# Optimization experiments

Hardware: AMD Instinct MI355X
Metric: run time of the kernel (lower is better)

Reference implementation:

```python
import jax, jax.numpy as jnp
import numpy as np

H = 128   # LSTM hidden size
E = 300   # embedding dim
PAD_ID = 0
UNK_ID = 1


def _lstm_dir(x, Wih, Whh, b):
    """Single-direction LSTM. x: [B,S,E] -> hidden states [B,S,H]. PyTorch gate order i,f,g,o."""
    B = x.shape[0]
    def step(carry, xt):
        h, c = carry
        g = xt @ Wih.T + h @ Whh.T + b            # [B,4H]
        i, f, gg, o = jnp.split(g, 4, axis=-1)
        c = jax.nn.sigmoid(f) * c + jax.nn.sigmoid(i) * jnp.tanh(gg)
        h = jax.nn.sigmoid(o) * jnp.tanh(c)
        return (h, c), h
    init = (jnp.zeros((B, H), x.dtype), jnp.zeros((B, H), x.dtype))
    _, hs = jax.lax.scan(step, init, jnp.swapaxes(x, 0, 1))   # [S,B,H]
    return jnp.swapaxes(hs, 0, 1)


def setup_inputs() -> dict:
    key = jax.random.key(0)
    ks = jax.random.split(key, 12)
    B, S, D = 32, 512, 8
    WORD_V, DEP_V, NUM_LABELS = 100000, 64, 5
    inp = {
        "word_ids": jax.random.randint(ks[0], (B, 3, S), 0, WORD_V, dtype=jnp.int32),
        "deps_ids": jax.random.randint(ks[1], (B, S, D), 0, DEP_V, dtype=jnp.int32),
        "word_table": jax.random.normal(ks[2], (WORD_V, E), jnp.float32) * 0.1,
        "dep_table": jax.random.normal(ks[3], (DEP_V, E), jnp.float32) * 0.1,
        "Wih_f": jax.random.normal(ks[4], (4 * H, E), jnp.float32) * 0.05,
        "Whh_f": jax.random.normal(ks[5], (4 * H, H), jnp.float32) * 0.05,
        "b_f": jnp.zeros((4 * H,), jnp.float32),
        "Wih_b": jax.random.normal(ks[6], (4 * H, E), jnp.float32) * 0.05,
        "Whh_b": jax.random.normal(ks[7], (4 * H, H), jnp.float32) * 0.05,
        "b_b": jnp.zeros((4 * H,), jnp.float32),
        "W_cls": jax.random.normal(ks[8], (NUM_LABELS, 2 * H), jnp.float32) * 0.05,
        "b_cls": jnp.zeros((NUM_LABELS,), jnp.float32),
    }
    return inp


def reference(word_ids, deps_ids, word_table, dep_table,
              Wih_f, Whh_f, b_f, Wih_b, Whh_b, b_b, W_cls, b_cls):
    # word_ids[:, 1, :] -> token ids used for word embeddings
    word_embs = word_table[word_ids[:, 1, :]]          # [B,S,E]
    dep_embs = dep_table[deps_ids]                     # [B,S,D,E]

    # vectorized masked mean-pool of dep embeddings (skip pad/unk ids)
    mask = ((deps_ids != PAD_ID) & (deps_ids != UNK_ID)).astype(word_embs.dtype)[..., None]  # [B,S,D,1]
    cnt = mask.sum(axis=2)                             # [B,S,1]
    dep_mean = (dep_embs * mask).sum(axis=2) / jnp.maximum(cnt, 1.0)
    word_embs = jnp.where(cnt > 0, 0.5 * word_embs + 0.5 * dep_mean, word_embs)

    # BiLSTM
    out_f = _lstm_dir(word_embs, Wih_f, Whh_f, b_f)                       # [B,S,H]
    out_b = _lstm_dir(word_embs[:, ::-1, :], Wih_b, Whh_b, b_b)[:, ::-1, :]
    out = jnp.concatenate([out_f, out_b], axis=-1)                        # [B,S,2H]

    # max-pool over time, dropout is identity in eval, then classifier
    pooled = out.max(axis=1)                           # [B,2H]
    logits = pooled @ W_cls.T + b_cls                  # [B,num_labels]
    return logits
```

## Files before the change

### kernel.cpp

```cpp
#include <hip/hip_runtime.h>
#include <hip/hip_bf16.h>
#include <cstdint>
#include <cstddef>

#define S_LEN 512
#define BATCH 32
#define EDIM  300
#define KPAD  320
#define K3    960
#define HDIM  128
#define NGATE 512
#define NCOLS 1024

typedef float    f2  __attribute__((ext_vector_type(2)));
typedef float    f4v __attribute__((ext_vector_type(4)));
typedef short    short8 __attribute__((ext_vector_type(8)));
typedef _Float16 h2  __attribute__((ext_vector_type(2)));

__device__ __forceinline__ float sigm_fast(float x) {
    return __builtin_amdgcn_rcpf(1.f + __expf(-x));
}
__device__ __forceinline__ float tanh_fast(float x) {
    return 2.f * sigm_fast(2.f * x) - 1.f;
}

template <int CTRL>
__device__ __forceinline__ float dpp_mov(float x) {
    int r = __builtin_amdgcn_update_dpp(0, __float_as_int(x), CTRL, 0xF, 0xF, true);
    return __int_as_float(r);
}

__device__ __forceinline__ h2 pk_f16(float a, float b) {
    auto r = __builtin_amdgcn_cvt_pkrtz(a, b);
    return __builtin_bit_cast(h2, r);
}

__device__ __forceinline__ void bf16_split(float v, ushort& hi, ushort& lo) {
    __hip_bfloat16 hb = __float2bfloat16(v);
    float hf = __bfloat162float(hb);
    __hip_bfloat16 lb = __float2bfloat16(v - hf);
    hi = *reinterpret_cast<ushort*>(&hb);
    lo = *reinterpret_cast<ushort*>(&lb);
}

__global__ void embed_xcat(const int* __restrict__ word_ids,
                           const int* __restrict__ deps_ids,
                           const float* __restrict__ word_table,
                           const float* __restrict__ dep_table,
                           ushort* __restrict__ Xcat) {
    int pos = blockIdx.x;
    int b = pos >> 9, s = pos & (S_LEN - 1);
    int wid = word_ids[b * 3 * S_LEN + S_LEN + s];
    const int* dp = deps_ids + (size_t)pos * 8;
    int ids[8];
    int cnt = 0;
#pragma unroll
    for (int d = 0; d < 8; ++d) {
        int id = dp[d];
        ids[d] = id;
        cnt += (id != 0 && id != 1) ? 1 : 0;
    }
    float inv = 0.5f / (float)((cnt > 0) ? cnt : 1);
    const float* wr = word_table + (size_t)wid * EDIM;
    ushort* xr = Xcat + (size_t)pos * K3;
    for (int e = threadIdx.x; e < KPAD; e += 128) {
        float v = 0.f;
        if (e < EDIM) {
            float w = wr[e];
            float dsum = 0.f;
#pragma unroll
            for (int d = 0; d < 8; ++d) {
                if (ids[d] != 0 && ids[d] != 1) dsum += dep_table[ids[d] * EDIM + e];
            }
            v = (cnt > 0) ? (0.5f * w + dsum * inv) : w;
        }
        ushort hu, lu;
        bf16_split(v, hu, lu);
        xr[e] = hu;
        xr[KPAD + e] = hu;
        xr[2 * KPAD + e] = lu;
    }
}

__global__ void wcat_kernel(const float* __restrict__ Wih_f,
                            const float* __restrict__ Wih_b,
                            ushort* __restrict__ Wcat) {
    int n = blockIdx.x;
    const float* src = (n < NGATE) ? (Wih_f + (size_t)n * EDIM)
                                   : (Wih_b + (size_t)(n - NGATE) * EDIM);
    ushort* wr = Wcat + (size_t)n * K3;
    for (int e = threadIdx.x; e < KPAD; e += 128) {
        float v = (e < EDIM) ? src[e] : 0.f;
        ushort hu, lu;
        bf16_split(v, hu, lu);
        wr[e] = hu;
        wr[KPAD + e] = lu;
        wr[2 * KPAD + e] = hu;
    }
}

#define LSTR 40
__global__ __launch_bounds__(256) void gemm_mfma(
        const ushort* __restrict__ Xcat,
        const ushort* __restrict__ Wcat,
        const float* __restrict__ b_f, const float* __restrict__ b_b,
        float* __restrict__ pre) {
    __shared__ ushort Asub[128 * LSTR];
    __shared__ ushort Bsub[128 * LSTR];
    int tid = threadIdx.x;
    int wave = tid >> 6, lane = tid & 63;
    int lid = lane & 15, quad = lane >> 4;
    int m0 = blockIdx.x * 128, n0 = blockIdx.y * 128;
    int wm = (wave >> 1) * 64, wn = (wave & 1) * 64;

    f4v acc[4][4];
#pragma unroll
    for (int i = 0; i < 4; ++i)
#pragma unroll
        for (int j = 0; j < 4; ++j) acc[i][j] = (f4v)0.f;

    float bias[4];
#pragma unroll
    for (int nt = 0; nt < 4; ++nt) {
        int n = n0 + wn + nt * 16 + lid;
        bias[nt] = (n < NGATE) ? b_f[n] : b_b[n - NGATE];
    }

    int c0 = tid, c1 = tid + 256;
    const ushort* aptr0 = Xcat + (size_t)(m0 + (c0 >> 2)) * K3 + (c0 & 3) * 8;
    const ushort* aptr1 = Xcat + (size_t)(m0 + (c1 >> 2)) * K3 + (c1 & 3) * 8;
    const ushort* bptr0 = Wcat + (size_t)(n0 + (c0 >> 2)) * K3 + (c0 & 3) * 8;
    const ushort* bptr1 = Wcat + (size_t)(n0 + (c1 >> 2)) * K3 + (c1 & 3) * 8;
    int la0 = (c0 >> 2) * LSTR + (c0 & 3) * 8;
    int la1 = (c1 >> 2) * LSTR + (c1 & 3) * 8;

    short8 ra0 = *(const short8*)(aptr0);
    short8 ra1 = *(const short8*)(aptr1);
    short8 rb0 = *(const short8*)(bptr0);
    short8 rb1 = *(const short8*)(bptr1);

    for (int k0 = 0; k0 < K3; k0 += 32) {
        __syncthreads();
        *(short8*)&Asub[la0] = ra0;
        *(short8*)&Asub[la1] = ra1;
        *(short8*)&Bsub[la0] = rb0;
        *(short8*)&Bsub[la1] = rb1;
        __syncthreads();
        if (k0 + 32 < K3) {
            ra0 = *(const short8*)(aptr0 + k0 + 32);
            ra1 = *(const short8*)(aptr1 + k0 + 32);
            rb0 = *(const short8*)(bptr0 + k0 + 32);
            rb1 = *(const short8*)(bptr1 + k0 + 32);
        }
        short8 aF[4], bF[4];
#pragma unroll
        for (int mt = 0; mt < 4; ++mt)
            aF[mt] = *(const short8*)&Asub[(wm + mt * 16 + lid) * LSTR + quad * 8];
#pragma unroll
        for (int nt = 0; nt < 4; ++nt)
            bF[nt] = *(const short8*)&Bsub[(wn + nt * 16 + lid) * LSTR + quad * 8];
#pragma unroll
        for (int mt = 0; mt < 4; ++mt)
#pragma unroll
            for (int nt = 0; nt < 4; ++nt)
                acc[mt][nt] = __builtin_amdgcn_mfma_f32_16x16x32_bf16(
                    aF[mt], bF[nt], acc[mt][nt], 0, 0, 0);
    }

#pragma unroll
    for (int mt = 0; mt < 4; ++mt)
#pragma unroll
        for (int nt = 0; nt < 4; ++nt) {
            int n = n0 + wn + nt * 16 + lid;
#pragma unroll
            for (int r = 0; r < 4; ++r) {
                int m = m0 + wm + mt * 16 + quad * 4 + r;
                pre[(size_t)m * NCOLS + n] = acc[mt][nt][r] + bias[nt];
            }
        }
}

__global__ __launch_bounds__(256, 1) void lstm_rec(
        const float* __restrict__ pre,
        const float* __restrict__ Whh_f, const float* __restrict__ Whh_b,
        float* __restrict__ pooled) {
    __shared__ _Float16 h_s[HDIM];
    int t = threadIdx.x;
    int lane = t & 63;
    int wv = t >> 6;
    int tau = lane & 3;
    int hx0 = wv * 16 + (lane >> 2);
    int hx1 = hx0 + 64;
    int b = blockIdx.x >> 1;
    int dir = blockIdx.x & 1;
    const float* Whh = dir ? Whh_b : Whh_f;

    h2 w0[64], w1[64];
    {
        const float* r0 = Whh + (size_t)(tau * HDIM + hx0) * HDIM;
        const float* r1 = Whh + (size_t)(tau * HDIM + hx1) * HDIM;
#pragma unroll
        for (int q = 0; q < 64; ++q) {
            w0[q] = pk_f16(r0[2 * q], r0[2 * q + 1]);
            w1[q] = pk_f16(r1[2 * q], r1[2 * q + 1]);
        }
    }

    float c0 = 0.f, c1 = 0.f;
    float hmax0 = -1e30f, hmax1 = -1e30f;
    if (t < 64) ((uint*)h_s)[t] = 0u;

    const float* pb0 = pre + (size_t)b * S_LEN * NCOLS + dir * NGATE + tau * HDIM + hx0;
    const float* pb1 = pb0 + 64;
    int s = dir ? (S_LEN - 1) : 0;
    int ds = dir ? -1 : 1;
    float p0n1 = pb0[(long)s * NCOLS];
    float p1n1 = pb1[(long)s * NCOLS];
    float p0n2 = pb0[(long)(s + ds) * NCOLS];
    float p1n2 = pb1[(long)(s + ds) * NCOLS];

    asm volatile("s_waitcnt lgkmcnt(0)\n\ts_barrier" ::: "memory");

    for (int step = 0; step < S_LEN; ++step) {
        float cur0 = p0n1, cur1 = p1n1;
        p0n1 = p0n2; p1n1 = p1n2;
        if (step + 2 < S_LEN) {
            p0n2 = pb0[(long)(s + 2 * ds) * NCOLS];
            p1n2 = pb1[(long)(s + 2 * ds) * NCOLS];
        }

        h2 hh[64];
        const h2* hp = (const h2*)h_s;
#pragma unroll
        for (int q = 0; q < 64; ++q) hh[q] = hp[q];

        float a0 = 0.f, a1 = 0.f, a2 = 0.f, a3 = 0.f;
        float e0 = 0.f, e1 = 0.f, e2 = 0.f, e3 = 0.f;
#pragma unroll
        for (int q = 0; q < 64; q += 4) {
            a0 = __builtin_amdgcn_fdot2(w0[q + 0], hh[q + 0], a0, false);
            a1 = __builtin_amdgcn_fdot2(w0[q + 1], hh[q + 1], a1, false);
            a2 = __builtin_amdgcn_fdot2(w0[q + 2], hh[q + 2], a2, false);
            a3 = __builtin_amdgcn_fdot2(w0[q + 3], hh[q + 3], a3, false);
            e0 = __builtin_amdgcn_fdot2(w1[q + 0], hh[q + 0], e0, false);
            e1 = __builtin_amdgcn_fdot2(w1[q + 1], hh[q + 1], e1, false);
            e2 = __builtin_amdgcn_fdot2(w1[q + 2], hh[q + 2], e2, false);
            e3 = __builtin_amdgcn_fdot2(w1[q + 3], hh[q + 3], e3, false);
        }
        float g0 = cur0 + (a0 + a1) + (a2 + a3);
        float g1 = cur1 + (e0 + e1) + (e2 + e3);

        float gi0 = dpp_mov<0x00>(g0), gf0 = dpp_mov<0x55>(g0);
        float gg0 = dpp_mov<0xAA>(g0), go0 = dpp_mov<0xFF>(g0);
        float gi1 = dpp_mov<0x00>(g1), gf1 = dpp_mov<0x55>(g1);
        float gg1 = dpp_mov<0xAA>(g1), go1 = dpp_mov<0xFF>(g1);

        c0 = sigm_fast(gf0) * c0 + sigm_fast(gi0) * tanh_fast(gg0);
        float h0 = sigm_fast(go0) * tanh_fast(c0);
        c1 = sigm_fast(gf1) * c1 + sigm_fast(gi1) * tanh_fast(gg1);
        float h1 = sigm_fast(go1) * tanh_fast(c1);
        hmax0 = fmaxf(hmax0, h0);
        hmax1 = fmaxf(hmax1, h1);

        if (tau == 0) {
            h_s[hx0] = (_Float16)h0;
            h_s[hx1] = (_Float16)h1;
        }
        asm volatile("s_waitcnt lgkmcnt(0)\n\ts_barrier" ::: "memory");
        s += ds;
    }

    if (tau == 0) {
        pooled[b * 256 + dir * HDIM + hx0] = hmax0;
        pooled[b * 256 + dir * HDIM + hx1] = hmax1;
    }
}

__global__ void cls_kernel(const float* __restrict__ pooled,
                           const float* __restrict__ W_cls,
                           const float* __restrict__ b_cls,
                           float* __restrict__ out) {
    int i = threadIdx.x;
    if (i < BATCH * 5) {
        int b = i / 5, l = i % 5;
        float acc = b_cls[l];
        const float* p = pooled + b * 256;
        const float* w = W_cls + l * 256;
#pragma unroll 8
        for (int j = 0; j < 256; ++j) acc = fmaf(p[j], w[j], acc);
        out[i] = acc;
    }
}

extern "C" void kernel_launch(void* const* d_in, const int* in_sizes, int n_in,
                              void* d_out, int out_size, void* d_ws, size_t ws_size,
                              hipStream_t stream) {
    const int*   word_ids   = (const int*)d_in[0];
    const int*   deps_ids   = (const int*)d_in[1];
    const float* word_table = (const float*)d_in[2];
    const float* dep_table  = (const float*)d_in[3];
    const float* Wih_f      = (const float*)d_in[4];
    const float* Whh_f      = (const float*)d_in[5];
    const float* b_f        = (const float*)d_in[6];
    const float* Wih_b      = (const float*)d_in[7];
    const float* Whh_b      = (const float*)d_in[8];
    const float* b_b        = (const float*)d_in[9];
    const float* W_cls      = (const float*)d_in[10];
    const float* b_cls      = (const float*)d_in[11];
    float* out = (float*)d_out;

    float*  pre    = (float*)d_ws;
    float*  pooled = pre + (size_t)BATCH * S_LEN * NCOLS;
    ushort* Xcat   = (ushort*)(pooled + BATCH * 256);
    ushort* Wcat   = Xcat + (size_t)BATCH * S_LEN * K3;

    embed_xcat<<<BATCH * S_LEN, 128, 0, stream>>>(word_ids, deps_ids,
                                                  word_table, dep_table, Xcat);
    wcat_kernel<<<NCOLS, 128, 0, stream>>>(Wih_f, Wih_b, Wcat);
    gemm_mfma<<<dim3(128, 8), 256, 0, stream>>>(Xcat, Wcat, b_f, b_b, pre);
    lstm_rec<<<64, 256, 0, stream>>>(pre, Whh_f, Whh_b, pooled);
    cls_kernel<<<1, 192, 0, stream>>>(pooled, W_cls, b_cls, out);
}
```

Baseline: 597.2 us.

## Split LSTM recurrent dot products across lanes with DPP reduction

Restructures the recurrent matvec so each lane handles a quarter of the K dimension for 8 hidden rows. Partial sums are combined with DPP row shifts and a select, instead of each lane doing a full 128-length dot product for 2 rows. This cuts per-lane LDS reads of h from 64 to 16 h2 and shortens the serial dot-product chain on the critical path of each step. In exchange it adds DPP reduction and select overhead, and the gate nonlinearities are now computed redundantly across lanes.

```diff
diff --git a/kernel.cpp b/kernel.cpp
--- a/kernel.cpp
+++ b/kernel.cpp
@@ -189,91 +189,99 @@
     int lane = t & 63;
     int wv = t >> 6;
     int tau = lane & 3;
-    int hx0 = wv * 16 + (lane >> 2);
-    int hx1 = hx0 + 64;
+    int ks  = (lane >> 2) & 3;
+    int hi2 = lane >> 4;
+    int hbase = wv * 32 + hi2 * 8;
     int b = blockIdx.x >> 1;
     int dir = blockIdx.x & 1;
     const float* Whh = dir ? Whh_b : Whh_f;
 
-    h2 w0[64], w1[64];
-    {
-        const float* r0 = Whh + (size_t)(tau * HDIM + hx0) * HDIM;
-        const float* r1 = Whh + (size_t)(tau * HDIM + hx1) * HDIM;
-#pragma unroll
-        for (int q = 0; q < 64; ++q) {
-            w0[q] = pk_f16(r0[2 * q], r0[2 * q + 1]);
-            w1[q] = pk_f16(r1[2 * q], r1[2 * q + 1]);
-        }
-    }
-
-    float c0 = 0.f, c1 = 0.f;
-    float hmax0 = -1e30f, hmax1 = -1e30f;
+    h2 w[8][16];
+#pragma unroll
+    for (int j = 0; j < 8; ++j) {
+        const float* rp = Whh + (size_t)(tau * HDIM + hbase + j) * HDIM + ks * 32;
+#pragma unroll
+        for (int q = 0; q < 16; ++q) w[j][q] = pk_f16(rp[2 * q], rp[2 * q + 1]);
+    }
+
+    float c = 0.f;
+    float hmax = -1e30f;
     if (t < 64) ((uint*)h_s)[t] = 0u;
 
-    const float* pb0 = pre + (size_t)b * S_LEN * NCOLS + dir * NGATE + tau * HDIM + hx0;
-    const float* pb1 = pb0 + 64;
+    const float* pX = pre + (size_t)b * S_LEN * NCOLS + dir * NGATE
+                    + tau * HDIM + hbase + 2 * ks;
+    const float* pY = pX + 1;
     int s = dir ? (S_LEN - 1) : 0;
-    int ds = dir ? -1 : 1;
-    float p0n1 = pb0[(long)s * NCOLS];
-    float p1n1 = pb1[(long)s * NCOLS];
-    float p0n2 = pb0[(long)(s + ds) * NCOLS];
-    float p1n2 = pb1[(long)(s + ds) * NCOLS];
+    int sd = dir ? -1 : 1;
+    float pXn1 = pX[(long)s * NCOLS], pYn1 = pY[(long)s * NCOLS];
+    float pXn2 = pX[(long)(s + sd) * NCOLS], pYn2 = pY[(long)(s + sd) * NCOLS];
+
+    int hZ = hbase + 2 * ks + (tau >> 1);
 
     asm volatile("s_waitcnt lgkmcnt(0)\n\ts_barrier" ::: "memory");
 
     for (int step = 0; step < S_LEN; ++step) {
-        float cur0 = p0n1, cur1 = p1n1;
-        p0n1 = p0n2; p1n1 = p1n2;
+        float curX = pXn1, curY = pYn1;
+        pXn1 = pXn2; pYn1 = pYn2;
         if (step + 2 < S_LEN) {
-            p0n2 = pb0[(long)(s + 2 * ds) * NCOLS];
-            p1n2 = pb1[(long)(s + 2 * ds) * NCOLS];
-        }
-
-        h2 hh[64];
+            pXn2 = pX[(long)(s + 2 * sd) * NCOLS];
+            pYn2 = pY[(long)(s + 2 * sd) * NCOLS];
+        }
+
+        h2 hh[16];
         const h2* hp = (const h2*)h_s;
 #pragma unroll
-        for (int q = 0; q < 64; ++q) hh[q] = hp[q];
-
-        float a0 = 0.f, a1 = 0.f, a2 = 0.f, a3 = 0.f;
-        float e0 = 0.f, e1 = 0.f, e2 = 0.f, e3 = 0.f;
-#pragma unroll
-        for (int q = 0; q < 64; q += 4) {
-            a0 = __builtin_amdgcn_fdot2(w0[q + 0], hh[q + 0], a0, false);
-            a1 = __builtin_amdgcn_fdot2(w0[q + 1], hh[q + 1], a1, false);
-            a2 = __builtin_amdgcn_fdot2(w0[q + 2], hh[q + 2], a2, false);
-            a3 = __builtin_amdgcn_fdot2(w0[q + 3], hh[q + 3], a3, false);
-            e0 = __builtin_amdgcn_fdot2(w1[q + 0], hh[q + 0], e0, false);
-            e1 = __builtin_amdgcn_fdot2(w1[q + 1], hh[q + 1], e1, false);
-            e2 = __builtin_amdgcn_fdot2(w1[q + 2], hh[q + 2], e2, false);
-            e3 = __builtin_amdgcn_fdot2(w1[q + 3], hh[q + 3], e3, false);
-        }
-        float g0 = cur0 + (a0 + a1) + (a2 + a3);
-        float g1 = cur1 + (e0 + e1) + (e2 + e3);
-
-        float gi0 = dpp_mov<0x00>(g0), gf0 = dpp_mov<0x55>(g0);
-        float gg0 = dpp_mov<0xAA>(g0), go0 = dpp_mov<0xFF>(g0);
-        float gi1 = dpp_mov<0x00>(g1), gf1 = dpp_mov<0x55>(g1);
-        float gg1 = dpp_mov<0xAA>(g1), go1 = dpp_mov<0xFF>(g1);
-
-        c0 = sigm_fast(gf0) * c0 + sigm_fast(gi0) * tanh_fast(gg0);
-        float h0 = sigm_fast(go0) * tanh_fast(c0);
-        c1 = sigm_fast(gf1) * c1 + sigm_fast(gi1) * tanh_fast(gg1);
-        float h1 = sigm_fast(go1) * tanh_fast(c1);
-        hmax0 = fmaxf(hmax0, h0);
-        hmax1 = fmaxf(hmax1, h1);
-
-        if (tau == 0) {
-            h_s[hx0] = (_Float16)h0;
-            h_s[hx1] = (_Float16)h1;
-        }
+        for (int q = 0; q < 16; ++q) hh[q] = hp[ks * 16 + q];
+
+        float P[8];
+#pragma unroll
+        for (int j = 0; j < 8; ++j) {
+            float acc = 0.f;
+#pragma unroll
+            for (int q = 0; q < 16; ++q)
+                acc = __builtin_amdgcn_fdot2(w[j][q], hh[q], acc, false);
+            P[j] = acc;
+        }
+
+        float R[8];
+#pragma unroll
+        for (int j = 0; j < 8; ++j) {
+            float r = P[j];
+            r += dpp_mov<0x124>(r);
+            r += dpp_mov<0x128>(r);
+            R[j] = r;
+        }
+
+        float X01 = (ks & 1) ? R[2] : R[0];
+        float X23 = (ks & 1) ? R[6] : R[4];
+        float X   = (ks & 2) ? X23 : X01;
+        float Y01 = (ks & 1) ? R[3] : R[1];
+        float Y23 = (ks & 1) ? R[7] : R[5];
+        float Y   = (ks & 2) ? Y23 : Y01;
+        float gX = X + curX;
+        float gY = Y + curY;
+
+        float giX = dpp_mov<0x00>(gX), gfX = dpp_mov<0x55>(gX);
+        float ggX = dpp_mov<0xAA>(gX), goX = dpp_mov<0xFF>(gX);
+        float giY = dpp_mov<0x00>(gY), gfY = dpp_mov<0x55>(gY);
+        float ggY = dpp_mov<0xAA>(gY), goY = dpp_mov<0xFF>(gY);
+
+        bool oy = (tau & 2) != 0;
+        float gi = oy ? giY : giX;
+        float gf = oy ? gfY : gfX;
+        float gg = oy ? ggY : ggX;
+        float go = oy ? goY : goX;
+
+        c = sigm_fast(gf) * c + sigm_fast(gi) * tanh_fast(gg);
+        float h = sigm_fast(go) * tanh_fast(c);
+        hmax = fmaxf(hmax, h);
+
+        if ((tau & 1) == 0) h_s[hZ] = (_Float16)h;
         asm volatile("s_waitcnt lgkmcnt(0)\n\ts_barrier" ::: "memory");
-        s += ds;
-    }
-
-    if (tau == 0) {
-        pooled[b * 256 + dir * HDIM + hx0] = hmax0;
-        pooled[b * 256 + dir * HDIM + hx1] = hmax1;
-    }
+        s += sd;
+    }
+
+    if ((tau & 1) == 0) pooled[b * 256 + dir * HDIM + hZ] = hmax;
 }
 
 __global__ void cls_kernel(const float* __restrict__ pooled,
```

Measured after the change: 514.5 us. 1.16x faster.
